# Kernel tuning notes

Measured on AMD Instinct MI355X. Metric: run time of the kernel, lower is better.

The kernel has to match this reference:

```python
import jax, jax.numpy as jnp
import numpy as np

D_MODEL = 1024
N_HEADS = 16
D_HEAD = D_MODEL // N_HEADS


def setup_inputs() -> dict:
    key = jax.random.key(0)
    k_x, k_qkv, k_proj = jax.random.split(key, 3)
    x = jax.random.normal(k_x, (4, 2048, D_MODEL), dtype=jnp.float32)
    # nn.Linear(d_model, 3*d_model, bias=False): weight shape [3*d_model, d_model]
    scale = 1.0 / np.sqrt(D_MODEL)
    W_qkv = jax.random.uniform(k_qkv, (3 * D_MODEL, D_MODEL), dtype=jnp.float32, minval=-scale, maxval=scale)
    W_proj = jax.random.uniform(k_proj, (D_MODEL, D_MODEL), dtype=jnp.float32, minval=-scale, maxval=scale)
    return {"x": x, "W_qkv": W_qkv, "W_proj": W_proj}


def reference(x, W_qkv, W_proj):
    B, T, C = x.shape
    qkv = jnp.einsum('btc,fc->btf', x, W_qkv)  # [B,T,3C]
    q, k, v = jnp.split(qkv, 3, axis=-1)
    # [B,T,H,Dh] -> [B,H,T,Dh]
    q = q.reshape(B, T, N_HEADS, D_HEAD).transpose(0, 2, 1, 3)
    k = k.reshape(B, T, N_HEADS, D_HEAD).transpose(0, 2, 1, 3)
    v = v.reshape(B, T, N_HEADS, D_HEAD).transpose(0, 2, 1, 3)
    att = jnp.einsum('bhqd,bhkd->bhqk', q, k) / jnp.sqrt(jnp.float32(D_HEAD))
    att = jax.nn.softmax(att, axis=-1)
    y = jnp.einsum('bhqk,bhkd->bhqd', att, v)
    y = y.transpose(0, 2, 1, 3).reshape(B, T, C)
    return jnp.einsum('btc,oc->bto', y, W_proj)
```

## Files before the change

### kernel.cpp

```cpp
#include <hip/hip_runtime.h>
#include <stdint.h>
#include <stddef.h>

#define SEQ   2048
#define NH    16
#define DH    64
#define DM    1024
#define NTOK  8192

typedef unsigned short u16;
typedef unsigned int u32;
typedef short bf16x8 __attribute__((ext_vector_type(8)));
typedef float f32x4  __attribute__((ext_vector_type(4)));
typedef unsigned short u16x4 __attribute__((ext_vector_type(4)));

#define QSCALE 0.18033688011112042f

#define WAIT_VM4 0x0F74
#define WAIT_VM0 0x0F70

__device__ __forceinline__ u16 f2bf(float f) {
  union { float f; unsigned u; } v; v.f = f;
  return (u16)((v.u + 0x7FFFu + ((v.u >> 16) & 1u)) >> 16);
}

__device__ __forceinline__ void gload_lds16(const void* g, void* l) {
  __builtin_amdgcn_global_load_lds(
      (const __attribute__((address_space(1))) void*)g,
      (__attribute__((address_space(3))) void*)l, 16, 0, 0);
}

__global__ __launch_bounds__(256) void cast_kernel(const float* __restrict__ src,
                                                   u16* __restrict__ dst, int n4) {
  int i = blockIdx.x * 256 + threadIdx.x;
  if (i < n4) {
    const float4 f = ((const float4*)src)[i];
    u16x4 o;
    o.x = f2bf(f.x); o.y = f2bf(f.y); o.z = f2bf(f.z); o.w = f2bf(f.w);
    ((u16x4*)dst)[i] = o;
  }
}

template <int EPI>
__global__ __launch_bounds__(256) void gemm_bt(
    const u16* __restrict__ A, const u16* __restrict__ B, int K_, int N_,
    u16* __restrict__ Qo, u16* __restrict__ Ko, u16* __restrict__ Vto,
    float* __restrict__ Co) {
  __shared__ __align__(16) u16 sA[128 * 64];
  __shared__ __align__(16) u16 sB[128 * 64];
  const int tid = threadIdx.x;
  const int wave = tid >> 6, lane = tid & 63;
  const int l16 = lane & 15, quad = lane >> 4;
  const int sw = l16 & 7;
  const int wm = (wave >> 1) * 64, wn = (wave & 1) * 64;
  const int row0 = blockIdx.y * 128, col0 = blockIdx.x * 128;
  const int ck0 = ((quad ^ sw) << 3);
  const int ck1 = (((quad + 4) ^ sw) << 3);

  f32x4 acc[4][4];
  for (int a = 0; a < 4; ++a)
    for (int b = 0; b < 4; ++b) acc[a][b] = (f32x4){0.f, 0.f, 0.f, 0.f};

  for (int k0 = 0; k0 < K_; k0 += 64) {
    __syncthreads();
    for (int j = 0; j < 4; ++j) {
      const int li = j * 256 + tid;
      const int r = li >> 3;
      const int cs = (((li & 7) ^ (r & 7)) << 3);
      gload_lds16(A + (size_t)(row0 + r) * K_ + k0 + cs, (char*)sA + li * 16);
      gload_lds16(B + (size_t)(col0 + r) * K_ + k0 + cs, (char*)sB + li * 16);
    }
    __syncthreads();
    for (int kk = 0; kk < 2; ++kk) {
      const int cko = kk ? ck1 : ck0;
      bf16x8 af[4], bfr[4];
      for (int i = 0; i < 4; ++i)
        af[i] = *(const bf16x8*)&sA[(wm + i * 16 + l16) * 64 + cko];
      for (int i = 0; i < 4; ++i)
        bfr[i] = *(const bf16x8*)&sB[(wn + i * 16 + l16) * 64 + cko];
      for (int mi = 0; mi < 4; ++mi)
        for (int ni = 0; ni < 4; ++ni)
          acc[mi][ni] = __builtin_amdgcn_mfma_f32_16x16x32_bf16(
              af[mi], bfr[ni], acc[mi][ni], 0, 0, 0);
    }
  }

  if (EPI == 0) {
    const int which = col0 >> 10;
    for (int mi = 0; mi < 4; ++mi)
      for (int ni = 0; ni < 4; ++ni) {
        const int rowb = row0 + wm + mi * 16 + quad * 4;
        const int col = col0 + wn + ni * 16 + l16;
        const int b = rowb >> 11, t = rowb & (SEQ - 1);
        const int c = col & (DM - 1);
        const int h = c >> 6, d = c & 63;
        const size_t bh = (size_t)b * NH + h;
        if (which == 2) {
          u16x4 pk;
          pk.x = f2bf(acc[mi][ni][0]); pk.y = f2bf(acc[mi][ni][1]);
          pk.z = f2bf(acc[mi][ni][2]); pk.w = f2bf(acc[mi][ni][3]);
          *(u16x4*)&Vto[(bh * DH + d) * SEQ + t] = pk;
        } else {
          for (int r = 0; r < 4; ++r) {
            const float v = acc[mi][ni][r];
            if (which == 0) Qo[(bh * SEQ + t + r) * DH + d] = f2bf(v * QSCALE);
            else            Ko[(bh * SEQ + t + r) * DH + d] = f2bf(v);
          }
        }
      }
  } else {
    for (int mi = 0; mi < 4; ++mi)
      for (int ni = 0; ni < 4; ++ni)
        for (int r = 0; r < 4; ++r) {
          const int row = row0 + wm + mi * 16 + quad * 4 + r;
          const int col = col0 + wn + ni * 16 + l16;
          Co[(size_t)row * N_ + col] = acc[mi][ni][r];
        }
  }
}

#define PSTRIDE 72
__global__ __launch_bounds__(256) void flash_attn(
    const u16* __restrict__ Q, const u16* __restrict__ Kk,
    const u16* __restrict__ Vt, u16* __restrict__ Y) {
  __shared__ __align__(16) u16 sK[2][64 * 64];
  __shared__ __align__(16) u16 sV[2][64 * 64];
  __shared__ __align__(16) u16 sP[4 * 32 * PSTRIDE];
  const int tid = threadIdx.x, wave = tid >> 6, lane = tid & 63;
  const int l16 = lane & 15, quad = lane >> 4;
  const int sw = l16 & 7;
  const int ck0 = ((quad ^ sw) << 3);
  const int ck1 = (((quad + 4) ^ sw) << 3);
  const int rloc = tid >> 3;
  const int cs = (((tid & 7) ^ (rloc & 7)) << 3);
  const int bh = blockIdx.y;
  const int q0 = blockIdx.x * 128 + wave * 32;
  const size_t qkBase = (size_t)bh * SEQ * DH;
  const size_t vtBase = (size_t)bh * DH * SEQ;

  bf16x8 qf[2][2];
  for (int ms = 0; ms < 2; ++ms) {
    const u16* qrow = Q + qkBase + (size_t)(q0 + ms * 16 + l16) * DH;
    qf[ms][0] = *(const bf16x8*)(qrow + quad * 8);
    qf[ms][1] = *(const bf16x8*)(qrow + 32 + quad * 8);
  }

  bf16x8 onesf;
  for (int i = 0; i < 8; ++i) onesf[i] = (short)0x3F80;

  f32x4 o[2][4];
  f32x4 osum[2];
  for (int a = 0; a < 2; ++a) {
    osum[a] = (f32x4){0.f, 0.f, 0.f, 0.f};
    for (int b = 0; b < 4; ++b) o[a][b] = (f32x4){0.f, 0.f, 0.f, 0.f};
  }

  u16* myP = sP + wave * 32 * PSTRIDE;
  const int pw0 = (0 * 16 + l16) * PSTRIDE;
  const int pw1 = (1 * 16 + l16) * PSTRIDE;

  for (int j = 0; j < 2; ++j) {
    const int r = j * 32 + rloc;
    gload_lds16(Kk + qkBase + (size_t)r * DH + cs, (char*)sK[0] + (j * 256 + tid) * 16);
    gload_lds16(Vt + vtBase + (size_t)r * SEQ + cs, (char*)sV[0] + (j * 256 + tid) * 16);
  }
  for (int t = 0; t < 32; ++t) {
    const int cur = t & 1;
    const int kt1 = ((t + 1) & 31) * 64;
    for (int j = 0; j < 2; ++j) {
      const int r = j * 32 + rloc;
      gload_lds16(Kk + qkBase + (size_t)(kt1 + r) * DH + cs, (char*)sK[cur ^ 1] + (j * 256 + tid) * 16);
      gload_lds16(Vt + vtBase + (size_t)r * SEQ + kt1 + cs, (char*)sV[cur ^ 1] + (j * 256 + tid) * 16);
    }
    __builtin_amdgcn_s_waitcnt(WAIT_VM4);
    __builtin_amdgcn_s_barrier();
    const u16* sk = sK[cur];
    const u16* sv = sV[cur];

    for (int nt = 0; nt < 4; ++nt) {
      bf16x8 kf0 = *(const bf16x8*)&sk[(nt * 16 + l16) * 64 + ck0];
      bf16x8 kf1 = *(const bf16x8*)&sk[(nt * 16 + l16) * 64 + ck1];
      for (int ms = 0; ms < 2; ++ms) {
        f32x4 st = (f32x4){0.f, 0.f, 0.f, 0.f};
        st = __builtin_amdgcn_mfma_f32_16x16x32_bf16(kf0, qf[ms][0], st, 0, 0, 0);
        st = __builtin_amdgcn_mfma_f32_16x16x32_bf16(kf1, qf[ms][1], st, 0, 0, 0);
        const u32 u0 = __builtin_bit_cast(u32, __builtin_amdgcn_exp2f(st[0]));
        const u32 u1 = __builtin_bit_cast(u32, __builtin_amdgcn_exp2f(st[1]));
        const u32 u2 = __builtin_bit_cast(u32, __builtin_amdgcn_exp2f(st[2]));
        const u32 u3 = __builtin_bit_cast(u32, __builtin_amdgcn_exp2f(st[3]));
        uint2 pk;
        pk.x = __builtin_amdgcn_perm(u1, u0, 0x07060302u);
        pk.y = __builtin_amdgcn_perm(u3, u2, 0x07060302u);
        *(uint2*)&myP[(ms ? pw1 : pw0) + nt * 16 + quad * 4] = pk;
      }
    }

    bf16x8 pf[2][2];
    pf[0][0] = *(const bf16x8*)&myP[pw0 + quad * 8];
    pf[0][1] = *(const bf16x8*)&myP[pw0 + 32 + quad * 8];
    pf[1][0] = *(const bf16x8*)&myP[pw1 + quad * 8];
    pf[1][1] = *(const bf16x8*)&myP[pw1 + 32 + quad * 8];
    for (int ms = 0; ms < 2; ++ms) {
      osum[ms] = __builtin_amdgcn_mfma_f32_16x16x32_bf16(pf[ms][0], onesf, osum[ms], 0, 0, 0);
      osum[ms] = __builtin_amdgcn_mfma_f32_16x16x32_bf16(pf[ms][1], onesf, osum[ms], 0, 0, 0);
    }
    for (int ds = 0; ds < 4; ++ds) {
      bf16x8 vf0 = *(const bf16x8*)&sv[(ds * 16 + l16) * 64 + ck0];
      bf16x8 vf1 = *(const bf16x8*)&sv[(ds * 16 + l16) * 64 + ck1];
      for (int ms = 0; ms < 2; ++ms) {
        o[ms][ds] = __builtin_amdgcn_mfma_f32_16x16x32_bf16(pf[ms][0], vf0, o[ms][ds], 0, 0, 0);
        o[ms][ds] = __builtin_amdgcn_mfma_f32_16x16x32_bf16(pf[ms][1], vf1, o[ms][ds], 0, 0, 0);
      }
    }
    __builtin_amdgcn_s_barrier();
  }
  __builtin_amdgcn_s_waitcnt(WAIT_VM0);

  float rl[2][4];
  for (int ms = 0; ms < 2; ++ms)
    for (int r = 0; r < 4; ++r)
      rl[ms][r] = __frcp_rn(osum[ms][r]);

  const int b = bh >> 4, h = bh & (NH - 1);
  for (int ms = 0; ms < 2; ++ms)
    for (int ds = 0; ds < 4; ++ds)
      for (int r = 0; r < 4; ++r) {
        const int t = q0 + ms * 16 + quad * 4 + r;
        const int d = ds * 16 + l16;
        Y[((size_t)(b * SEQ + t)) * DM + h * DH + d] = f2bf(o[ms][ds][r] * rl[ms][r]);
      }
}

extern "C" void kernel_launch(void* const* d_in, const int* in_sizes, int n_in,
                              void* d_out, int out_size, void* d_ws, size_t ws_size,
                              hipStream_t stream) {
  const float* x     = (const float*)d_in[0];
  const float* Wqkv  = (const float*)d_in[1];
  const float* Wproj = (const float*)d_in[2];
  float* out = (float*)d_out;

  u16* xb    = (u16*)d_ws;
  u16* wqkvb = xb + (size_t)NTOK * DM;
  u16* wprojb = wqkvb + (size_t)3 * DM * DM;
  u16* Qb  = wprojb + (size_t)DM * DM;
  u16* Kb  = Qb + (size_t)NTOK * DM;
  u16* Vtb = Kb + (size_t)NTOK * DM;
  u16* Yb  = Vtb + (size_t)NTOK * DM;

  {
    int n4 = NTOK * DM / 4;
    cast_kernel<<<(n4 + 255) / 256, 256, 0, stream>>>(x, xb, n4);
    n4 = 3 * DM * DM / 4;
    cast_kernel<<<(n4 + 255) / 256, 256, 0, stream>>>(Wqkv, wqkvb, n4);
    n4 = DM * DM / 4;
    cast_kernel<<<(n4 + 255) / 256, 256, 0, stream>>>(Wproj, wprojb, n4);
  }

  gemm_bt<0><<<dim3(3 * DM / 128, NTOK / 128), 256, 0, stream>>>(
      xb, wqkvb, DM, 3 * DM, Qb, Kb, Vtb, nullptr);

  flash_attn<<<dim3(SEQ / 128, 4 * NH), 256, 0, stream>>>(Qb, Kb, Vtb, Yb);

  gemm_bt<1><<<dim3(DM / 128, NTOK / 128), 256, 0, stream>>>(
      Yb, wprojb, DM, DM, nullptr, nullptr, nullptr, out);
}
```

Baseline: 290.0 us.

## Pre-pack GEMM weights into MFMA fragment layout, double-buffer A, enlarge attention query tiles

Weights are now cast and packed by a new kernel into a fragment-major layout, so each wave loads its B operands straight from global memory into registers and B no longer goes through LDS. The A tile is double-buffered in LDS, with the next tile prefetched through async loads and a partial waitcnt before each step. Flash attention now gives each wave 64 query rows instead of 32, which reuses every K/V tile over more rows and halves the grid. The costs are more VGPRs for the register-resident B fragments and the larger accumulators, which may lower occupancy, and fewer attention blocks in flight.

```diff
diff --git a/kernel.cpp b/kernel.cpp
--- a/kernel.cpp
+++ b/kernel.cpp
@@ -13,11 +13,13 @@
 typedef short bf16x8 __attribute__((ext_vector_type(8)));
 typedef float f32x4  __attribute__((ext_vector_type(4)));
 typedef unsigned short u16x4 __attribute__((ext_vector_type(4)));
+typedef unsigned short u16x8 __attribute__((ext_vector_type(8)));
 
 #define QSCALE 0.18033688011112042f
 
-#define WAIT_VM4 0x0F74
-#define WAIT_VM0 0x0F70
+#define WAIT_VM12 0x0F7C
+#define WAIT_VM4  0x0F74
+#define WAIT_VM0  0x0F70
 
 __device__ __forceinline__ u16 f2bf(float f) {
   union { float f; unsigned u; } v; v.f = f;
@@ -41,13 +43,27 @@
   }
 }
 
+__global__ __launch_bounds__(256) void pack_b(const float* __restrict__ W,
+                                              u16* __restrict__ Bp, int NS) {
+  const int chunk = blockIdx.x * 256 + threadIdx.x;
+  const int lane = chunk & 63, blk = chunk >> 6;
+  const int c = blk / NS, s = blk % NS;
+  const int n = s * 16 + (lane & 15);
+  const int k0 = c * 32 + (lane >> 4) * 8;
+  const float4 f0 = *(const float4*)&W[(size_t)n * DM + k0];
+  const float4 f1 = *(const float4*)&W[(size_t)n * DM + k0 + 4];
+  u16x8 o;
+  o[0] = f2bf(f0.x); o[1] = f2bf(f0.y); o[2] = f2bf(f0.z); o[3] = f2bf(f0.w);
+  o[4] = f2bf(f1.x); o[5] = f2bf(f1.y); o[6] = f2bf(f1.z); o[7] = f2bf(f1.w);
+  *(u16x8*)&Bp[(size_t)chunk * 8] = o;
+}
+
 template <int EPI>
-__global__ __launch_bounds__(256) void gemm_bt(
-    const u16* __restrict__ A, const u16* __restrict__ B, int K_, int N_,
+__global__ __launch_bounds__(256) void gemm_flat(
+    const u16* __restrict__ A, const u16* __restrict__ Bp, int NS, int N_,
     u16* __restrict__ Qo, u16* __restrict__ Ko, u16* __restrict__ Vto,
     float* __restrict__ Co) {
-  __shared__ __align__(16) u16 sA[128 * 64];
-  __shared__ __align__(16) u16 sB[128 * 64];
+  __shared__ __align__(16) u16 sA[2][128 * 64];
   const int tid = threadIdx.x;
   const int wave = tid >> 6, lane = tid & 63;
   const int l16 = lane & 15, quad = lane >> 4;
@@ -56,34 +72,59 @@
   const int row0 = blockIdx.y * 128, col0 = blockIdx.x * 128;
   const int ck0 = ((quad ^ sw) << 3);
   const int ck1 = (((quad + 4) ^ sw) << 3);
+  const int scol = (col0 + wn) >> 4;
+  const u16* bpw = Bp + (size_t)lane * 8;
 
   f32x4 acc[4][4];
   for (int a = 0; a < 4; ++a)
     for (int b = 0; b < 4; ++b) acc[a][b] = (f32x4){0.f, 0.f, 0.f, 0.f};
 
-  for (int k0 = 0; k0 < K_; k0 += 64) {
-    __syncthreads();
+  bf16x8 bfr[2][2][4];
+
+  for (int j = 0; j < 4; ++j) {
+    const int li = j * 256 + tid;
+    const int r = li >> 3;
+    const int cs = (((li & 7) ^ (r & 7)) << 3);
+    gload_lds16(A + (size_t)(row0 + r) * DM + cs, (char*)sA[0] + li * 16);
+  }
+  for (int kk = 0; kk < 2; ++kk) {
+    const u16* bb = bpw + ((size_t)kk * NS + scol) * 512;
+    for (int i = 0; i < 4; ++i)
+      bfr[0][kk][i] = *(const bf16x8*)(bb + i * 512);
+  }
+
+#pragma unroll 2
+  for (int t = 0; t < 16; ++t) {
+    const int cur = t & 1;
+    const int tn = (t + 1) & 15;
+    const int k1 = tn << 6;
     for (int j = 0; j < 4; ++j) {
       const int li = j * 256 + tid;
       const int r = li >> 3;
       const int cs = (((li & 7) ^ (r & 7)) << 3);
-      gload_lds16(A + (size_t)(row0 + r) * K_ + k0 + cs, (char*)sA + li * 16);
-      gload_lds16(B + (size_t)(col0 + r) * K_ + k0 + cs, (char*)sB + li * 16);
-    }
-    __syncthreads();
+      gload_lds16(A + (size_t)(row0 + r) * DM + k1 + cs, (char*)sA[cur ^ 1] + li * 16);
+    }
+    for (int kk = 0; kk < 2; ++kk) {
+      const u16* bb = bpw + ((size_t)(tn * 2 + kk) * NS + scol) * 512;
+      for (int i = 0; i < 4; ++i)
+        bfr[cur ^ 1][kk][i] = *(const bf16x8*)(bb + i * 512);
+    }
+    __builtin_amdgcn_s_waitcnt(WAIT_VM12);
+    __builtin_amdgcn_s_barrier();
+    const u16* sa = sA[cur];
     for (int kk = 0; kk < 2; ++kk) {
       const int cko = kk ? ck1 : ck0;
-      bf16x8 af[4], bfr[4];
+      bf16x8 af[4];
       for (int i = 0; i < 4; ++i)
-        af[i] = *(const bf16x8*)&sA[(wm + i * 16 + l16) * 64 + cko];
-      for (int i = 0; i < 4; ++i)
-        bfr[i] = *(const bf16x8*)&sB[(wn + i * 16 + l16) * 64 + cko];
+        af[i] = *(const bf16x8*)&sa[(wm + i * 16 + l16) * 64 + cko];
       for (int mi = 0; mi < 4; ++mi)
         for (int ni = 0; ni < 4; ++ni)
           acc[mi][ni] = __builtin_amdgcn_mfma_f32_16x16x32_bf16(
-              af[mi], bfr[ni], acc[mi][ni], 0, 0, 0);
-    }
-  }
+              af[mi], bfr[cur][kk][ni], acc[mi][ni], 0, 0, 0);
+    }
+    __builtin_amdgcn_s_barrier();
+  }
+  __builtin_amdgcn_s_waitcnt(WAIT_VM0);
 
   if (EPI == 0) {
     const int which = col0 >> 10;
@@ -125,7 +166,7 @@
     const u16* __restrict__ Vt, u16* __restrict__ Y) {
   __shared__ __align__(16) u16 sK[2][64 * 64];
   __shared__ __align__(16) u16 sV[2][64 * 64];
-  __shared__ __align__(16) u16 sP[4 * 32 * PSTRIDE];
+  __shared__ __align__(16) u16 sP[4 * 64 * PSTRIDE];
   const int tid = threadIdx.x, wave = tid >> 6, lane = tid & 63;
   const int l16 = lane & 15, quad = lane >> 4;
   const int sw = l16 & 7;
@@ -134,12 +175,12 @@
   const int rloc = tid >> 3;
   const int cs = (((tid & 7) ^ (rloc & 7)) << 3);
   const int bh = blockIdx.y;
-  const int q0 = blockIdx.x * 128 + wave * 32;
+  const int q0 = blockIdx.x * 256 + wave * 64;
   const size_t qkBase = (size_t)bh * SEQ * DH;
   const size_t vtBase = (size_t)bh * DH * SEQ;
 
-  bf16x8 qf[2][2];
-  for (int ms = 0; ms < 2; ++ms) {
+  bf16x8 qf[4][2];
+  for (int ms = 0; ms < 4; ++ms) {
     const u16* qrow = Q + qkBase + (size_t)(q0 + ms * 16 + l16) * DH;
     qf[ms][0] = *(const bf16x8*)(qrow + quad * 8);
     qf[ms][1] = *(const bf16x8*)(qrow + 32 + quad * 8);
@@ -148,16 +189,14 @@
   bf16x8 onesf;
   for (int i = 0; i < 8; ++i) onesf[i] = (short)0x3F80;
 
-  f32x4 o[2][4];
-  f32x4 osum[2];
-  for (int a = 0; a < 2; ++a) {
+  f32x4 o[4][4];
+  f32x4 osum[4];
+  for (int a = 0; a < 4; ++a) {
     osum[a] = (f32x4){0.f, 0.f, 0.f, 0.f};
     for (int b = 0; b < 4; ++b) o[a][b] = (f32x4){0.f, 0.f, 0.f, 0.f};
   }
 
-  u16* myP = sP + wave * 32 * PSTRIDE;
-  const int pw0 = (0 * 16 + l16) * PSTRIDE;
-  const int pw1 = (1 * 16 + l16) * PSTRIDE;
+  u16* myP = sP + wave * 64 * PSTRIDE;
 
   for (int j = 0; j < 2; ++j) {
     const int r = j * 32 + rloc;
@@ -180,7 +219,7 @@
     for (int nt = 0; nt < 4; ++nt) {
       bf16x8 kf0 = *(const bf16x8*)&sk[(nt * 16 + l16) * 64 + ck0];
       bf16x8 kf1 = *(const bf16x8*)&sk[(nt * 16 + l16) * 64 + ck1];
-      for (int ms = 0; ms < 2; ++ms) {
+      for (int ms = 0; ms < 4; ++ms) {
         f32x4 st = (f32x4){0.f, 0.f, 0.f, 0.f};
         st = __builtin_amdgcn_mfma_f32_16x16x32_bf16(kf0, qf[ms][0], st, 0, 0, 0);
         st = __builtin_amdgcn_mfma_f32_16x16x32_bf16(kf1, qf[ms][1], st, 0, 0, 0);
@@ -191,23 +230,23 @@
         uint2 pk;
         pk.x = __builtin_amdgcn_perm(u1, u0, 0x07060302u);
         pk.y = __builtin_amdgcn_perm(u3, u2, 0x07060302u);
-        *(uint2*)&myP[(ms ? pw1 : pw0) + nt * 16 + quad * 4] = pk;
+        *(uint2*)&myP[(ms * 16 + l16) * PSTRIDE + nt * 16 + quad * 4] = pk;
       }
     }
 
-    bf16x8 pf[2][2];
-    pf[0][0] = *(const bf16x8*)&myP[pw0 + quad * 8];
-    pf[0][1] = *(const bf16x8*)&myP[pw0 + 32 + quad * 8];
-    pf[1][0] = *(const bf16x8*)&myP[pw1 + quad * 8];
-    pf[1][1] = *(const bf16x8*)&myP[pw1 + 32 + quad * 8];
-    for (int ms = 0; ms < 2; ++ms) {
+    bf16x8 pf[4][2];
+    for (int ms = 0; ms < 4; ++ms) {
+      pf[ms][0] = *(const bf16x8*)&myP[(ms * 16 + l16) * PSTRIDE + quad * 8];
+      pf[ms][1] = *(const bf16x8*)&myP[(ms * 16 + l16) * PSTRIDE + 32 + quad * 8];
+    }
+    for (int ms = 0; ms < 4; ++ms) {
       osum[ms] = __builtin_amdgcn_mfma_f32_16x16x32_bf16(pf[ms][0], onesf, osum[ms], 0, 0, 0);
       osum[ms] = __builtin_amdgcn_mfma_f32_16x16x32_bf16(pf[ms][1], onesf, osum[ms], 0, 0, 0);
     }
     for (int ds = 0; ds < 4; ++ds) {
       bf16x8 vf0 = *(const bf16x8*)&sv[(ds * 16 + l16) * 64 + ck0];
       bf16x8 vf1 = *(const bf16x8*)&sv[(ds * 16 + l16) * 64 + ck1];
-      for (int ms = 0; ms < 2; ++ms) {
+      for (int ms = 0; ms < 4; ++ms) {
         o[ms][ds] = __builtin_amdgcn_mfma_f32_16x16x32_bf16(pf[ms][0], vf0, o[ms][ds], 0, 0, 0);
         o[ms][ds] = __builtin_amdgcn_mfma_f32_16x16x32_bf16(pf[ms][1], vf1, o[ms][ds], 0, 0, 0);
       }
@@ -216,13 +255,13 @@
   }
   __builtin_amdgcn_s_waitcnt(WAIT_VM0);
 
-  float rl[2][4];
-  for (int ms = 0; ms < 2; ++ms)
+  float rl[4][4];
+  for (int ms = 0; ms < 4; ++ms)
     for (int r = 0; r < 4; ++r)
       rl[ms][r] = __frcp_rn(osum[ms][r]);
 
   const int b = bh >> 4, h = bh & (NH - 1);
-  for (int ms = 0; ms < 2; ++ms)
+  for (int ms = 0; ms < 4; ++ms)
     for (int ds = 0; ds < 4; ++ds)
       for (int r = 0; r < 4; ++r) {
         const int t = q0 + ms * 16 + quad * 4 + r;
@@ -239,10 +278,10 @@
   const float* Wproj = (const float*)d_in[2];
   float* out = (float*)d_out;
 
-  u16* xb    = (u16*)d_ws;
-  u16* wqkvb = xb + (size_t)NTOK * DM;
-  u16* wprojb = wqkvb + (size_t)3 * DM * DM;
-  u16* Qb  = wprojb + (size_t)DM * DM;
+  u16* xb     = (u16*)d_ws;
+  u16* bpQkv  = xb + (size_t)NTOK * DM;
+  u16* bpProj = bpQkv + (size_t)3 * DM * DM;
+  u16* Qb  = bpProj + (size_t)DM * DM;
   u16* Kb  = Qb + (size_t)NTOK * DM;
   u16* Vtb = Kb + (size_t)NTOK * DM;
   u16* Yb  = Vtb + (size_t)NTOK * DM;
@@ -250,17 +289,15 @@
   {
     int n4 = NTOK * DM / 4;
     cast_kernel<<<(n4 + 255) / 256, 256, 0, stream>>>(x, xb, n4);
-    n4 = 3 * DM * DM / 4;
-    cast_kernel<<<(n4 + 255) / 256, 256, 0, stream>>>(Wqkv, wqkvb, n4);
-    n4 = DM * DM / 4;
-    cast_kernel<<<(n4 + 255) / 256, 256, 0, stream>>>(Wproj, wprojb, n4);
-  }
-
-  gemm_bt<0><<<dim3(3 * DM / 128, NTOK / 128), 256, 0, stream>>>(
-      xb, wqkvb, DM, 3 * DM, Qb, Kb, Vtb, nullptr);
-
-  flash_attn<<<dim3(SEQ / 128, 4 * NH), 256, 0, stream>>>(Qb, Kb, Vtb, Yb);
-
-  gemm_bt<1><<<dim3(DM / 128, NTOK / 128), 256, 0, stream>>>(
-      Yb, wprojb, DM, DM, nullptr, nullptr, nullptr, out);
-}
+    pack_b<<<3 * DM * DM / 8 / 256, 256, 0, stream>>>(Wqkv, bpQkv, 3 * DM / 16);
+    pack_b<<<DM * DM / 8 / 256, 256, 0, stream>>>(Wproj, bpProj, DM / 16);
+  }
+
+  gemm_flat<0><<<dim3(3 * DM / 128, NTOK / 128), 256, 0, stream>>>(
+      xb, bpQkv, 3 * DM / 16, 3 * DM, Qb, Kb, Vtb, nullptr);
+
+  flash_attn<<<dim3(SEQ / 256, 4 * NH), 256, 0, stream>>>(Qb, Kb, Vtb, Yb);
+
+  gemm_flat<1><<<dim3(DM / 128, NTOK / 128), 256, 0, stream>>>(
+      Yb, bpProj, DM / 16, DM, nullptr, nullptr, nullptr, out);
+}
```

Measured after the change: 275.8 us. -4.9%, faster.
